# Kernel tuning notes

Measured on AMD Instinct MI355X. Metric: run time of the kernel, lower is better.

## Reference

```python
import jax, jax.numpy as jnp
from jax import lax
import numpy as np

VOCAB = 50000
E = 301  # 300-dim pretrained + appended ones column
D = 25
NUM_CLASSES = 5


def setup_inputs() -> dict:
    key = jax.random.key(0)
    ks = jax.random.split(key, 8)
    B, S = 2048, 128
    words = jax.random.randint(ks[0], (B, S), 0, VOCAB)
    emb = jax.random.normal(ks[1], (VOCAB, E - 1), dtype=jnp.float32)
    # hstack ones column as in __init__
    emb_table = jnp.concatenate([emb, jnp.ones((VOCAB, 1), jnp.float32)], axis=1)
    A = jax.random.normal(ks[2], (D, E, D), dtype=jnp.float32) * 0.02
    W = jax.random.normal(ks[3], (E, D), dtype=jnp.float32) * 0.02
    V = jax.random.normal(ks[4], (D, D), dtype=jnp.float32) * 0.02
    b = jax.random.normal(ks[5], (D,), dtype=jnp.float32) * 0.02
    out_W = jax.random.normal(ks[6], (NUM_CLASSES, D), dtype=jnp.float32) * 0.02
    out_b = jax.random.normal(ks[7], (NUM_CLASSES,), dtype=jnp.float32) * 0.02
    return {"words": words, "batch_size": B, "emb_table": emb_table,
            "A": A, "W": W, "V": V, "b": b, "out_W": out_W, "out_b": out_b}


def reference(words, batch_size, emb_table, A, W, V, b, out_W, out_b):
    x_seq = emb_table[words]                      # [B, S, E] frozen embedding gather
    h0 = jnp.zeros((batch_size, D), jnp.float32).at[:, -1].set(1.0)

    def step(h, x):  # x: [B, E], h: [B, D]
        # a[b,i] = sum_{e,j} x[b,e] A[i,e,j] h[b,j]  (bilinear tensor term)
        a = jnp.einsum('be,ied,bd->bi', x, A, h)
        lin = x @ W + h @ V + b
        return jnp.tanh(a + lin), None

    h, _ = lax.scan(step, h0, jnp.swapaxes(x_seq, 0, 1))  # scan over S
    logits = h @ out_W.T + out_b                 # [B, num_classes]
    return jax.nn.sigmoid(logits)
```

## Files before the change

kernel.cpp:

```cpp
#include <hip/hip_runtime.h>
#include <math.h>

#define VOCAB 50000
#define EE 301
#define DD 25
#define SEQ 128
#define NC 5
#define BROW 768
#define NUSE 700
#define TROW 704

__global__ __launch_bounds__(256) void build_B(
    const float* __restrict__ A, const float* __restrict__ W,
    float* __restrict__ Bmat)
{
    int e = blockIdx.x;
    for (int c = threadIdx.x; c < BROW; c += 256) {
        float v = 0.f;
        if (c < NUSE) {
            int i = c / 28, j = c % 28;
            if (j < 25)       v = A[((size_t)i * EE + e) * DD + j];
            else if (j == 25) v = W[(size_t)e * DD + i];
        }
        Bmat[(size_t)e * BROW + c] = v;
    }
}

__global__ __launch_bounds__(256, 2) void gemm_T(
    const float* __restrict__ emb,
    const float* __restrict__ Bmat,
    float* __restrict__ T)
{
    __shared__ float As[2][16][132];
    __shared__ float Bs[2][16][132];
    int tid = threadIdx.x;
    int tx = tid & 15, ty = tid >> 4;
    int m0 = blockIdx.x * 128;
    int n0 = blockIdx.y * 128;

    float acc[8][8];
#pragma unroll
    for (int a = 0; a < 8; ++a)
#pragma unroll
        for (int c = 0; c < 8; ++c) acc[a][c] = 0.f;

    float  ar[8];
    float4 br[2];
    int kl0 = tid >> 5, nl0 = (tid & 31) * 4;

#pragma unroll
    for (int it = 0; it < 8; ++it) {
        int m = m0 + ty + 16 * it, k = tx;
        ar[it] = (m < VOCAB && k < EE) ? emb[(size_t)m * EE + k] : 0.f;
    }
#pragma unroll
    for (int it = 0; it < 2; ++it) {
        int k = kl0 + 8 * it;
        br[it] = (k < EE) ? *(const float4*)(Bmat + (size_t)k * BROW + n0 + nl0)
                          : make_float4(0.f, 0.f, 0.f, 0.f);
    }
#pragma unroll
    for (int it = 0; it < 8; ++it) As[0][tx][ty + 16 * it] = ar[it];
#pragma unroll
    for (int it = 0; it < 2; ++it) *(float4*)(&Bs[0][kl0 + 8 * it][nl0]) = br[it];
    __syncthreads();

    int buf = 0;
    for (int k0 = 0; k0 < EE; k0 += 16) {
        int k1 = k0 + 16;
        bool more = (k1 < EE);
        if (more) {
#pragma unroll
            for (int it = 0; it < 8; ++it) {
                int m = m0 + ty + 16 * it, k = k1 + tx;
                ar[it] = (m < VOCAB && k < EE) ? emb[(size_t)m * EE + k] : 0.f;
            }
#pragma unroll
            for (int it = 0; it < 2; ++it) {
                int k = k1 + kl0 + 8 * it;
                br[it] = (k < EE) ? *(const float4*)(Bmat + (size_t)k * BROW + n0 + nl0)
                                  : make_float4(0.f, 0.f, 0.f, 0.f);
            }
        }
#pragma unroll
        for (int kk = 0; kk < 16; ++kk) {
            float4 a0 = *(const float4*)&As[buf][kk][ty * 4];
            float4 a1 = *(const float4*)&As[buf][kk][64 + ty * 4];
            float4 b0 = *(const float4*)&Bs[buf][kk][tx * 4];
            float4 b1 = *(const float4*)&Bs[buf][kk][64 + tx * 4];
            float av[8] = {a0.x, a0.y, a0.z, a0.w, a1.x, a1.y, a1.z, a1.w};
            float bv[8] = {b0.x, b0.y, b0.z, b0.w, b1.x, b1.y, b1.z, b1.w};
#pragma unroll
            for (int a = 0; a < 8; ++a)
#pragma unroll
                for (int c = 0; c < 8; ++c)
                    acc[a][c] = fmaf(av[a], bv[c], acc[a][c]);
        }
        if (more) {
            int nb = buf ^ 1;
#pragma unroll
            for (int it = 0; it < 8; ++it) As[nb][tx][ty + 16 * it] = ar[it];
#pragma unroll
            for (int it = 0; it < 2; ++it) *(float4*)(&Bs[nb][kl0 + 8 * it][nl0]) = br[it];
            __syncthreads();
            buf = nb;
        }
    }

#pragma unroll
    for (int gi = 0; gi < 2; ++gi) {
#pragma unroll
        for (int r = 0; r < 4; ++r) {
            int m = m0 + gi * 64 + ty * 4 + r;
            if (m < VOCAB) {
                float* row = T + (size_t)m * TROW;
#pragma unroll
                for (int gc = 0; gc < 2; ++gc) {
                    int n = n0 + gc * 64 + tx * 4;
                    if (n < TROW) {
                        int a = gi * 4 + r, c = gc * 4;
                        *(float4*)(row + n) = make_float4(
                            acc[a][c], acc[a][c + 1], acc[a][c + 2], acc[a][c + 3]);
                    }
                }
            }
        }
    }
}

__global__ __launch_bounds__(256) void rnn_scan_np4(
    const int*   __restrict__ words,
    const float* __restrict__ T,
    const float* __restrict__ V,
    const float* __restrict__ bvec,
    const float* __restrict__ outW,
    const float* __restrict__ outB,
    float* __restrict__ out,
    int B)
{
    int tid = threadIdx.x;
    int g = tid >> 5, i = tid & 31;
    int b = blockIdx.x * 8 + g;
    bool act = (i < DD) && (b < B);
    int ii = (i < DD) ? i : (DD - 1);
    int bsafe = (b < B) ? b : 0;
    const int* wr = words + (size_t)bsafe * SEQ;

    float Vcol[DD];
#pragma unroll
    for (int j = 0; j < DD; ++j) Vcol[j] = V[j * DD + ii];
    float bi = bvec[ii];

    float hr[DD];
#pragma unroll
    for (int j = 0; j < DD; ++j) hr[j] = 0.f;
    hr[DD - 1] = 1.f;

    bool sse = ((b & 3) == 0) && ((i & 3) == 0);
    const float* base = T + (size_t)ii * 28;

    float4 cur[7], nxt[7];
    {
        const float* R = base + (size_t)wr[0] * TROW;
#pragma unroll
        for (int u = 0; u < 7; ++u) cur[u] = *(const float4*)(R + u * 4);
    }

    float hnew = 0.f;
    for (int t = 0; t < SEQ; ++t) {
        int wn = wr[(t + 1 < SEQ) ? t + 1 : t];
        const float* Rn = base + (size_t)wn * TROW;
#pragma unroll
        for (int u = 0; u < 7; ++u) nxt[u] = *(const float4*)(Rn + u * 4);

        float Tj[28];
#pragma unroll
        for (int u = 0; u < 7; ++u) {
            Tj[u * 4 + 0] = cur[u].x; Tj[u * 4 + 1] = cur[u].y;
            Tj[u * 4 + 2] = cur[u].z; Tj[u * 4 + 3] = cur[u].w;
        }
        float qv = Tj[25];

        float a;
        if (sse) {
            float p0 = 0.f, p1 = 0.f, p2 = 0.f, p3 = 0.f;
#pragma unroll
            for (int j = 0; j < 24; j += 4) {
                p0 = __fadd_rn(p0, __fmul_rn(Tj[j],     hr[j]));
                p1 = __fadd_rn(p1, __fmul_rn(Tj[j + 1], hr[j + 1]));
                p2 = __fadd_rn(p2, __fmul_rn(Tj[j + 2], hr[j + 2]));
                p3 = __fadd_rn(p3, __fmul_rn(Tj[j + 3], hr[j + 3]));
            }
            float s02 = __fadd_rn(p0, p2);
            float s13 = __fadd_rn(p1, p3);
            a = __fadd_rn(s02, s13);
            a = __fadd_rn(a, __fmul_rn(Tj[24], hr[24]));
        } else {
            a = 0.f;
#pragma unroll
            for (int j = 0; j < DD; ++j)
                a = __fadd_rn(a, __fmul_rn(Tj[j], hr[j]));
        }

        float r2 = 0.f;
#pragma unroll
        for (int j = 0; j < DD; ++j)
            r2 = fmaf(hr[j], Vcol[j], r2);

        float lin = __fadd_rn(__fadd_rn(qv, r2), bi);
        float pre = __fadd_rn(a, lin);
        hnew = act ? (float)tanh((double)pre) : 0.f;

#pragma unroll
        for (int j = 0; j < DD; ++j)
            hr[j] = __shfl(hnew, j, 32);

#pragma unroll
        for (int u = 0; u < 7; ++u) cur[u] = nxt[u];
    }

    if (i < NC && b < B) {
        float acc = 0.f;
#pragma unroll
        for (int j = 0; j < DD; ++j)
            acc = fmaf(hr[j], outW[i * DD + j], acc);
        float l = __fadd_rn(acc, outB[i]);
        out[(size_t)b * NC + i] = (float)(1.0 / (1.0 + exp(-(double)l)));
    }
}

extern "C" void kernel_launch(void* const* d_in, const int* in_sizes, int n_in,
                              void* d_out, int out_size, void* d_ws, size_t ws_size,
                              hipStream_t stream)
{
    const int*   words = (const int*)d_in[0];
    const float* emb   = (const float*)d_in[2];
    const float* A     = (const float*)d_in[3];
    const float* W     = (const float*)d_in[4];
    const float* V     = (const float*)d_in[5];
    const float* bias  = (const float*)d_in[6];
    const float* outW  = (const float*)d_in[7];
    const float* outB  = (const float*)d_in[8];
    float* out = (float*)d_out;
    int B = in_sizes[0] / SEQ;

    float* Bmat = (float*)d_ws;
    float* T    = (float*)((char*)d_ws + (1 << 20));

    build_B<<<EE, 256, 0, stream>>>(A, W, Bmat);
    gemm_T<<<dim3((VOCAB + 127) / 128, 6), 256, 0, stream>>>(emb, Bmat, T);
    rnn_scan_np4<<<(B + 7) / 8, 256, 0, stream>>>(words, T, V, bias, outW, outB, out, B);
}
```

Measured before the change: 512.0 us.

## Transpose embedding table and use direct global-to-LDS loads in vocab GEMM

```diff
diff --git a/kernel.cpp b/kernel.cpp
--- a/kernel.cpp
+++ b/kernel.cpp
@@ -3,12 +3,18 @@
 
 #define VOCAB 50000
 #define EE 301
+#define KP 304
 #define DD 25
 #define SEQ 128
 #define NC 5
 #define BROW 768
 #define NUSE 700
 #define TROW 704
+#define EMT 50048
+
+#define GLOAD_LDS16(g, l) __builtin_amdgcn_global_load_lds( \
+    (const __attribute__((address_space(1))) void*)(g),     \
+    (__attribute__((address_space(3))) void*)(l), 16, 0, 0)
 
 __global__ __launch_bounds__(256) void build_B(
     const float* __restrict__ A, const float* __restrict__ W,
@@ -17,7 +23,7 @@
     int e = blockIdx.x;
     for (int c = threadIdx.x; c < BROW; c += 256) {
         float v = 0.f;
-        if (c < NUSE) {
+        if (e < EE && c < NUSE) {
             int i = c / 28, j = c % 28;
             if (j < 25)       v = A[((size_t)i * EE + e) * DD + j];
             else if (j == 25) v = W[(size_t)e * DD + i];
@@ -26,17 +32,40 @@
     }
 }
 
-__global__ __launch_bounds__(256, 2) void gemm_T(
-    const float* __restrict__ emb,
+__global__ __launch_bounds__(256) void transpose_emb(
+    const float* __restrict__ emb, float* __restrict__ embT)
+{
+    __shared__ float t[64][65];
+    int m0 = blockIdx.x * 64, k0 = blockIdx.y * 64;
+    int tx = threadIdx.x & 63, ty = threadIdx.x >> 6;
+#pragma unroll
+    for (int it = 0; it < 16; ++it) {
+        int m = m0 + ty * 16 + it;
+        int k = k0 + tx;
+        t[tx][ty * 16 + it] = (m < VOCAB && k < EE) ? emb[(size_t)m * EE + k] : 0.f;
+    }
+    __syncthreads();
+#pragma unroll
+    for (int it = 0; it < 16; ++it) {
+        int kl = ty * 16 + it;
+        int k = k0 + kl;
+        if (k < KP) embT[(size_t)k * EMT + m0 + tx] = t[kl][tx];
+    }
+}
+
+__global__ __launch_bounds__(256, 2) void gemm_T2(
+    const float* __restrict__ embT,
     const float* __restrict__ Bmat,
     float* __restrict__ T)
 {
-    __shared__ float As[2][16][132];
-    __shared__ float Bs[2][16][132];
+    __shared__ float As[2][16][128];
+    __shared__ float Bs[2][16][128];
     int tid = threadIdx.x;
     int tx = tid & 15, ty = tid >> 4;
-    int m0 = blockIdx.x * 128;
-    int n0 = blockIdx.y * 128;
+    int m0 = blockIdx.x * 128, n0 = blockIdx.y * 128;
+    int wave = tid >> 6, lane = tid & 63;
+    int krow = lane >> 5;
+    int col4 = (lane & 31) * 4;
 
     float acc[8][8];
 #pragma unroll
@@ -44,44 +73,22 @@
 #pragma unroll
         for (int c = 0; c < 8; ++c) acc[a][c] = 0.f;
 
-    float  ar[8];
-    float4 br[2];
-    int kl0 = tid >> 5, nl0 = (tid & 31) * 4;
-
-#pragma unroll
-    for (int it = 0; it < 8; ++it) {
-        int m = m0 + ty + 16 * it, k = tx;
-        ar[it] = (m < VOCAB && k < EE) ? emb[(size_t)m * EE + k] : 0.f;
-    }
-#pragma unroll
-    for (int it = 0; it < 2; ++it) {
-        int k = kl0 + 8 * it;
-        br[it] = (k < EE) ? *(const float4*)(Bmat + (size_t)k * BROW + n0 + nl0)
-                          : make_float4(0.f, 0.f, 0.f, 0.f);
-    }
-#pragma unroll
-    for (int it = 0; it < 8; ++it) As[0][tx][ty + 16 * it] = ar[it];
-#pragma unroll
-    for (int it = 0; it < 2; ++it) *(float4*)(&Bs[0][kl0 + 8 * it][nl0]) = br[it];
+    auto dma_tile = [&](int k0, int buf) {
+#pragma unroll
+        for (int j = 0; j < 2; ++j) {
+            int r0 = wave * 4 + j * 2;
+            int k = k0 + r0 + krow;
+            GLOAD_LDS16(embT + (size_t)k * EMT + m0 + col4, &As[buf][r0][0]);
+            GLOAD_LDS16(Bmat + (size_t)k * BROW + n0 + col4, &Bs[buf][r0][0]);
+        }
+    };
+
+    dma_tile(0, 0);
     __syncthreads();
 
     int buf = 0;
-    for (int k0 = 0; k0 < EE; k0 += 16) {
-        int k1 = k0 + 16;
-        bool more = (k1 < EE);
-        if (more) {
-#pragma unroll
-            for (int it = 0; it < 8; ++it) {
-                int m = m0 + ty + 16 * it, k = k1 + tx;
-                ar[it] = (m < VOCAB && k < EE) ? emb[(size_t)m * EE + k] : 0.f;
-            }
-#pragma unroll
-            for (int it = 0; it < 2; ++it) {
-                int k = k1 + kl0 + 8 * it;
-                br[it] = (k < EE) ? *(const float4*)(Bmat + (size_t)k * BROW + n0 + nl0)
-                                  : make_float4(0.f, 0.f, 0.f, 0.f);
-            }
-        }
+    for (int k0 = 0; k0 < KP; k0 += 16) {
+        if (k0 + 16 < KP) dma_tile(k0 + 16, buf ^ 1);
 #pragma unroll
         for (int kk = 0; kk < 16; ++kk) {
             float4 a0 = *(const float4*)&As[buf][kk][ty * 4];
@@ -96,15 +103,8 @@
                 for (int c = 0; c < 8; ++c)
                     acc[a][c] = fmaf(av[a], bv[c], acc[a][c]);
         }
-        if (more) {
-            int nb = buf ^ 1;
-#pragma unroll
-            for (int it = 0; it < 8; ++it) As[nb][tx][ty + 16 * it] = ar[it];
-#pragma unroll
-            for (int it = 0; it < 2; ++it) *(float4*)(&Bs[nb][kl0 + 8 * it][nl0]) = br[it];
-            __syncthreads();
-            buf = nb;
-        }
+        __syncthreads();
+        buf ^= 1;
     }
 
 #pragma unroll
@@ -128,7 +128,101 @@
     }
 }
 
-__global__ __launch_bounds__(256) void rnn_scan_np4(
+__global__ __launch_bounds__(256, 2) void gemm_T(
+    const float* __restrict__ emb, const float* __restrict__ Bmat,
+    float* __restrict__ T)
+{
+    __shared__ float As[2][16][132];
+    __shared__ float Bs[2][16][132];
+    int tid = threadIdx.x;
+    int tx = tid & 15, ty = tid >> 4;
+    int m0 = blockIdx.x * 128, n0 = blockIdx.y * 128;
+    float acc[8][8];
+#pragma unroll
+    for (int a = 0; a < 8; ++a)
+#pragma unroll
+        for (int c = 0; c < 8; ++c) acc[a][c] = 0.f;
+    float ar[8]; float4 br[2];
+    int kl0 = tid >> 5, nl0 = (tid & 31) * 4;
+#pragma unroll
+    for (int it = 0; it < 8; ++it) {
+        int m = m0 + ty + 16 * it, k = tx;
+        ar[it] = (m < VOCAB && k < EE) ? emb[(size_t)m * EE + k] : 0.f;
+    }
+#pragma unroll
+    for (int it = 0; it < 2; ++it) {
+        int k = kl0 + 8 * it;
+        br[it] = (k < EE) ? *(const float4*)(Bmat + (size_t)k * BROW + n0 + nl0)
+                          : make_float4(0.f, 0.f, 0.f, 0.f);
+    }
+#pragma unroll
+    for (int it = 0; it < 8; ++it) As[0][tx][ty + 16 * it] = ar[it];
+#pragma unroll
+    for (int it = 0; it < 2; ++it) *(float4*)(&Bs[0][kl0 + 8 * it][nl0]) = br[it];
+    __syncthreads();
+    int buf = 0;
+    for (int k0 = 0; k0 < EE; k0 += 16) {
+        int k1 = k0 + 16;
+        bool more = (k1 < EE);
+        if (more) {
+#pragma unroll
+            for (int it = 0; it < 8; ++it) {
+                int m = m0 + ty + 16 * it, k = k1 + tx;
+                ar[it] = (m < VOCAB && k < EE) ? emb[(size_t)m * EE + k] : 0.f;
+            }
+#pragma unroll
+            for (int it = 0; it < 2; ++it) {
+                int k = k1 + kl0 + 8 * it;
+                br[it] = (k < EE) ? *(const float4*)(Bmat + (size_t)k * BROW + n0 + nl0)
+                                  : make_float4(0.f, 0.f, 0.f, 0.f);
+            }
+        }
+#pragma unroll
+        for (int kk = 0; kk < 16; ++kk) {
+            float4 a0 = *(const float4*)&As[buf][kk][ty * 4];
+            float4 a1 = *(const float4*)&As[buf][kk][64 + ty * 4];
+            float4 b0 = *(const float4*)&Bs[buf][kk][tx * 4];
+            float4 b1 = *(const float4*)&Bs[buf][kk][64 + tx * 4];
+            float av[8] = {a0.x, a0.y, a0.z, a0.w, a1.x, a1.y, a1.z, a1.w};
+            float bv[8] = {b0.x, b0.y, b0.z, b0.w, b1.x, b1.y, b1.z, b1.w};
+#pragma unroll
+            for (int a = 0; a < 8; ++a)
+#pragma unroll
+                for (int c = 0; c < 8; ++c)
+                    acc[a][c] = fmaf(av[a], bv[c], acc[a][c]);
+        }
+        if (more) {
+            int nb = buf ^ 1;
+#pragma unroll
+            for (int it = 0; it < 8; ++it) As[nb][tx][ty + 16 * it] = ar[it];
+#pragma unroll
+            for (int it = 0; it < 2; ++it) *(float4*)(&Bs[nb][kl0 + 8 * it][nl0]) = br[it];
+            __syncthreads();
+            buf = nb;
+        }
+    }
+#pragma unroll
+    for (int gi = 0; gi < 2; ++gi) {
+#pragma unroll
+        for (int r = 0; r < 4; ++r) {
+            int m = m0 + gi * 64 + ty * 4 + r;
+            if (m < VOCAB) {
+                float* row = T + (size_t)m * TROW;
+#pragma unroll
+                for (int gc = 0; gc < 2; ++gc) {
+                    int n = n0 + gc * 64 + tx * 4;
+                    if (n < TROW) {
+                        int a = gi * 4 + r, c = gc * 4;
+                        *(float4*)(row + n) = make_float4(
+                            acc[a][c], acc[a][c + 1], acc[a][c + 2], acc[a][c + 3]);
+                    }
+                }
+            }
+        }
+    }
+}
+
+__global__ __launch_bounds__(256) void rnn_scan_np5(
     const int*   __restrict__ words,
     const float* __restrict__ T,
     const float* __restrict__ V,
@@ -159,28 +253,22 @@
     bool sse = ((b & 3) == 0) && ((i & 3) == 0);
     const float* base = T + (size_t)ii * 28;
 
-    float4 cur[7], nxt[7];
-    {
-        const float* R = base + (size_t)wr[0] * TROW;
-#pragma unroll
-        for (int u = 0; u < 7; ++u) cur[u] = *(const float4*)(R + u * 4);
-    }
+    float4 A0[7], A1[7], A2[7];
+    auto LD = [&](float4* dst, int t) {
+        const float* R = base + (size_t)wr[t] * TROW;
+#pragma unroll
+        for (int u = 0; u < 7; ++u) dst[u] = *(const float4*)(R + u * 4);
+    };
 
     float hnew = 0.f;
-    for (int t = 0; t < SEQ; ++t) {
-        int wn = wr[(t + 1 < SEQ) ? t + 1 : t];
-        const float* Rn = base + (size_t)wn * TROW;
-#pragma unroll
-        for (int u = 0; u < 7; ++u) nxt[u] = *(const float4*)(Rn + u * 4);
-
+    auto STEP = [&](const float4* C) {
         float Tj[28];
 #pragma unroll
         for (int u = 0; u < 7; ++u) {
-            Tj[u * 4 + 0] = cur[u].x; Tj[u * 4 + 1] = cur[u].y;
-            Tj[u * 4 + 2] = cur[u].z; Tj[u * 4 + 3] = cur[u].w;
+            Tj[u * 4 + 0] = C[u].x; Tj[u * 4 + 1] = C[u].y;
+            Tj[u * 4 + 2] = C[u].z; Tj[u * 4 + 3] = C[u].w;
         }
         float qv = Tj[25];
-
         float a;
         if (sse) {
             float p0 = 0.f, p1 = 0.f, p2 = 0.f, p3 = 0.f;
@@ -201,23 +289,27 @@
             for (int j = 0; j < DD; ++j)
                 a = __fadd_rn(a, __fmul_rn(Tj[j], hr[j]));
         }
-
         float r2 = 0.f;
 #pragma unroll
         for (int j = 0; j < DD; ++j)
             r2 = fmaf(hr[j], Vcol[j], r2);
-
         float lin = __fadd_rn(__fadd_rn(qv, r2), bi);
         float pre = __fadd_rn(a, lin);
         hnew = act ? (float)tanh((double)pre) : 0.f;
-
 #pragma unroll
         for (int j = 0; j < DD; ++j)
             hr[j] = __shfl(hnew, j, 32);
-
-#pragma unroll
-        for (int u = 0; u < 7; ++u) cur[u] = nxt[u];
-    }
+    };
+
+    LD(A0, 0);
+    LD(A1, 1);
+    for (int t = 0; t + 2 < SEQ; t += 3) {
+        LD(A2, t + 2); STEP(A0);
+        LD(A0, t + 3); STEP(A1);
+        LD(A1, t + 4); STEP(A2);
+    }
+    STEP(A0);
+    STEP(A1);
 
     if (i < NC && b < B) {
         float acc = 0.f;
@@ -244,10 +336,19 @@
     float* out = (float*)d_out;
     int B = in_sizes[0] / SEQ;
 
+    const size_t T_OFF    = (size_t)1 << 20;
+    const size_t EMBT_OFF = (size_t)144 << 20;
+    const size_t NEED     = EMBT_OFF + (size_t)KP * EMT * 4;
     float* Bmat = (float*)d_ws;
-    float* T    = (float*)((char*)d_ws + (1 << 20));
-
-    build_B<<<EE, 256, 0, stream>>>(A, W, Bmat);
-    gemm_T<<<dim3((VOCAB + 127) / 128, 6), 256, 0, stream>>>(emb, Bmat, T);
-    rnn_scan_np4<<<(B + 7) / 8, 256, 0, stream>>>(words, T, V, bias, outW, outB, out, B);
-}
+    float* T    = (float*)((char*)d_ws + T_OFF);
+    float* embT = (float*)((char*)d_ws + EMBT_OFF);
+
+    build_B<<<KP, 256, 0, stream>>>(A, W, Bmat);
+    if (ws_size >= NEED) {
+        transpose_emb<<<dim3(EMT / 64, (KP + 63) / 64), 256, 0, stream>>>(emb, embT);
+        gemm_T2<<<dim3((VOCAB + 127) / 128, 6), 256, 0, stream>>>(embT, Bmat, T);
+    } else {
+        gemm_T<<<dim3((VOCAB + 127) / 128, 6), 256, 0, stream>>>(emb, Bmat, T);
+    }
+    rnn_scan_np5<<<(B + 7) / 8, 256, 0, stream>>>(words, T, V, bias, outW, outB, out, B);
+}
```

Result: no change. 511.3 us (-0.1%).
